# Optimization experiments

Measured on AMD Instinct MI355X. Metric: run time of the kernel, lower is better.

Reference implementation:

```python
import jax, jax.numpy as jnp
import numpy as np

N = 100_000   # nodes
E = 3_200_000 # edges (avg degree 32)
D = 256       # gnn width
H = 128       # mlp hidden
C = 5         # num classes


def _gcn_conv(x, W, b, src, dst, norm, n):
    # PyG GCNConv: h = x @ W^T, then symmetric-normalized scatter-add over edges
    h = x @ W.T
    msgs = norm[:, None] * h[src]                      # [E+N, out]
    out = jax.ops.segment_sum(msgs, dst, num_segments=n)
    return out + b


def setup_inputs() -> dict:
    key = jax.random.key(0)
    ks = jax.random.split(key, 8)
    x = jax.random.normal(ks[0], (N, D), dtype=jnp.float32)
    edge_index = jax.random.randint(ks[1], (2, E), 0, N, dtype=jnp.int32)
    def lin(k, out_d, in_d):
        return jax.random.normal(k, (out_d, in_d), dtype=jnp.float32) / np.sqrt(in_d).astype(np.float32)
    return {
        "x": x,
        "edge_index": edge_index,
        "W1": lin(ks[2], D, D), "b1": jnp.zeros((D,), jnp.float32),
        "W2": lin(ks[3], D, D), "b2": jnp.zeros((D,), jnp.float32),
        "Wm1": lin(ks[4], H, D), "bm1": jnp.zeros((H,), jnp.float32),
        "Wm2": lin(ks[5], C, H), "bm2": jnp.zeros((C,), jnp.float32),
    }


def reference(x, edge_index, W1, b1, W2, b2, Wm1, bm1, Wm2, bm2):
    # add self-loops (PyG GCNConv default add_self_loops=True)
    loop = jnp.arange(N, dtype=edge_index.dtype)
    src = jnp.concatenate([edge_index[0], loop])
    dst = jnp.concatenate([edge_index[1], loop])
    # symmetric normalization: deg from destination index (flow source_to_target)
    deg = jax.ops.segment_sum(jnp.ones(src.shape[0], x.dtype), dst, num_segments=N)
    dinv = jnp.where(deg > 0, jax.lax.rsqrt(deg), 0.0)
    norm = dinv[src] * dinv[dst]                       # [E+N]

    h = _gcn_conv(x, W1, b1, src, dst, norm, N)
    h = _gcn_conv(h, W2, b2, src, dst, norm, N)
    # MLP head (no activations in original module)
    h = h @ Wm1.T + bm1
    h = h @ Wm2.T + bm2
    return h
```

## Files before the change

### kernel.cpp

```cpp
#include <hip/hip_runtime.h>

#define N_NODES 100000
#define N_EDGES 3200000
#define DIM 256
#define HID 128
#define NCLS 5
#define BSH 8
#define BSZ 256
#define NBUCK 391
#define P1B 256
#define EPB 12500
#define HPKC 16

__global__ void k_zero(int* p, int n) {
    int i = blockIdx.x * 256 + threadIdx.x;
    if (i < n) p[i] = 0;
}

template<int K>
__global__ __launch_bounds__(256) void k_hp_stage(const float* __restrict__ A,
        const float* __restrict__ B, float* __restrict__ OUT)
{
    int t = threadIdx.x;
    int k0 = blockIdx.x * HPKC;
    float acc[NCLS] = {0, 0, 0, 0, 0};
    #pragma unroll
    for (int kk = 0; kk < HPKC; ++kk) {
        int k = k0 + kk;
        float b = B[k * DIM + t];
        #pragma unroll
        for (int c = 0; c < NCLS; ++c) acc[c] += A[c * K + k] * b;
    }
    #pragma unroll
    for (int c = 0; c < NCLS; ++c) unsafeAtomicAdd(&OUT[c * DIM + t], acc[c]);
}

__global__ __launch_bounds__(320) void k_hp_bias(const float* __restrict__ Wc,
        const float* __restrict__ W2c, const float* __restrict__ Wm2,
        const float* __restrict__ b1, const float* __restrict__ b2,
        const float* __restrict__ bm1, const float* __restrict__ bm2,
        float* __restrict__ bq, float* __restrict__ bc2)
{
    int c = threadIdx.x >> 6;
    int lane = threadIdx.x & 63;
    float s = 0.0f;
    for (int i = lane; i < DIM; i += 64) s += W2c[c * DIM + i] * b1[i];
    #pragma unroll
    for (int off = 32; off > 0; off >>= 1) s += __shfl_xor(s, off);
    float b = 0.0f;
    for (int k = lane; k < HID; k += 64) b += Wm2[c * HID + k] * bm1[k];
    for (int o = lane; o < DIM; o += 64) b += Wc[c * DIM + o] * b2[o];
    #pragma unroll
    for (int off = 32; off > 0; off >>= 1) b += __shfl_xor(b, off);
    if (lane == 0) { bq[c] = s; bc2[c] = bm2[c] + b; }
}

__global__ __launch_bounds__(1024) void k_p1hist(const int* __restrict__ dst,
        int* __restrict__ gcount, int* __restrict__ blockbase)
{
    __shared__ int lh[NBUCK];
    int tid = threadIdx.x;
    for (int i = tid; i < NBUCK; i += 1024) lh[i] = 0;
    __syncthreads();
    int s = blockIdx.x * EPB, e1 = s + EPB;
    for (int e = s + tid; e < e1; e += 1024) atomicAdd(&lh[dst[e] >> BSH], 1);
    __syncthreads();
    for (int i = tid; i < NBUCK; i += 1024) {
        int c = lh[i];
        blockbase[blockIdx.x * NBUCK + i] = c ? atomicAdd(&gcount[i], c) : 0;
    }
}
__global__ __launch_bounds__(512) void k_scanb(const int* __restrict__ gcount,
        int* __restrict__ gbase)
{
    __shared__ int sdata[512];
    int tid = threadIdx.x;
    int v = (tid < NBUCK) ? gcount[tid] : 0;
    sdata[tid] = v;
    __syncthreads();
    #pragma unroll
    for (int off = 1; off < 512; off <<= 1) {
        int t = (tid >= off) ? sdata[tid - off] : 0;
        __syncthreads();
        sdata[tid] += t;
        __syncthreads();
    }
    if (tid < NBUCK) gbase[tid] = sdata[tid] - v;
    if (tid == 0) gbase[NBUCK] = N_EDGES;
}
__global__ __launch_bounds__(1024) void k_p1scatter(const int* __restrict__ src,
        const int* __restrict__ dst, const int* __restrict__ gbase,
        const int* __restrict__ blockbase, unsigned* __restrict__ ebuf)
{
    __shared__ int lh[NBUCK];
    int tid = threadIdx.x;
    for (int i = tid; i < NBUCK; i += 1024) lh[i] = 0;
    __syncthreads();
    int s = blockIdx.x * EPB, e1 = s + EPB;
    for (int e = s + tid; e < e1; e += 1024) {
        int d = dst[e];
        int b = d >> BSH;
        int r = atomicAdd(&lh[b], 1);
        int pos = gbase[b] + blockbase[blockIdx.x * NBUCK + b] + r;
        ebuf[pos] = ((unsigned)src[e] << 8) | (unsigned)(d & 255);
    }
}
__global__ __launch_bounds__(512) void k_p2(const unsigned* __restrict__ ebuf,
        const int* __restrict__ gbase, int* __restrict__ rowptr,
        float* __restrict__ dinv, int* __restrict__ esrc)
{
    __shared__ int c[BSZ];
    __shared__ int sdata[BSZ];
    __shared__ int cur[BSZ];
    int tid = threadIdx.x, b = blockIdx.x;
    if (tid < BSZ) c[tid] = 0;
    __syncthreads();
    int s = gbase[b], e1 = gbase[b + 1];
    for (int e = s + tid; e < e1; e += 512) atomicAdd(&c[ebuf[e] & 255u], 1);
    __syncthreads();
    int cnt = (tid < BSZ) ? c[tid] : 0;
    if (tid < BSZ) sdata[tid] = cnt;
    __syncthreads();
    #pragma unroll
    for (int off = 1; off < BSZ; off <<= 1) {
        int t = (tid >= off && tid < BSZ) ? sdata[tid - off] : 0;
        __syncthreads();
        if (tid < BSZ) sdata[tid] += t;
        __syncthreads();
    }
    if (tid < BSZ) {
        int rp = s + sdata[tid] - cnt;
        cur[tid] = rp;
        int node = b * BSZ + tid;
        if (node < N_NODES) {
            rowptr[node] = rp;
            dinv[node] = rsqrtf((float)(cnt + 1));
        }
    }
    if (b == 0 && tid == 0) rowptr[N_NODES] = N_EDGES;
    __syncthreads();
    for (int e = s + tid; e < e1; e += 512) {
        unsigned p = ebuf[e];
        int pos = atomicAdd(&cur[p & 255u], 1);
        esrc[pos] = (int)(p >> 8);
    }
}

__global__ __launch_bounds__(256) void k_q(const float* __restrict__ x,
        const float* __restrict__ Wq, const float* __restrict__ dinv,
        float* __restrict__ qbuf)
{
    int wid = (blockIdx.x * 256 + threadIdx.x) >> 6;
    int lane = threadIdx.x & 63;
    int lane4 = lane * 4;
    int nwaves = gridDim.x * 4;
    float4 w[NCLS];
    #pragma unroll
    for (int c = 0; c < NCLS; ++c) w[c] = *(const float4*)(Wq + c * DIM + lane4);
    for (int d = wid; d < N_NODES; d += nwaves) {
        float4 xv = *(const float4*)(x + (size_t)d * DIM + lane4);
        float p[NCLS];
        #pragma unroll
        for (int c = 0; c < NCLS; ++c) {
            float s = xv.x * w[c].x + xv.y * w[c].y + xv.z * w[c].z + xv.w * w[c].w;
            #pragma unroll
            for (int off = 32; off > 0; off >>= 1) s += __shfl_xor(s, off);
            p[c] = s;
        }
        if (lane == 0) {
            float dv = dinv[d];
            #pragma unroll
            for (int c = 0; c < NCLS; ++c) qbuf[(size_t)d * 8 + c] = dv * p[c];
        }
    }
}

template<int MODE>
__global__ __launch_bounds__(256) void k_gather5(const float* __restrict__ in,
        const int* __restrict__ rowptr, const int* __restrict__ esrc,
        const float* __restrict__ dinv, const float* __restrict__ bias,
        float* __restrict__ out, int ostride)
{
    int gid = blockIdx.x * 256 + threadIdx.x;
    int d = gid >> 2, sub = gid & 3;
    if (d >= N_NODES) return;
    float acc0 = 0, acc1 = 0, acc2 = 0, acc3 = 0, acc4 = 0;
    int r0 = rowptr[d], r1 = rowptr[d + 1];
    for (int j = r0 + sub; j < r1; j += 4) {
        int s = esrc[j];
        float4 v = *(const float4*)(in + (size_t)s * 8);
        float v4 = in[(size_t)s * 8 + 4];
        acc0 += v.x; acc1 += v.y; acc2 += v.z; acc3 += v.w; acc4 += v4;
    }
    if (sub == 0) {
        float4 v = *(const float4*)(in + (size_t)d * 8);
        float v4 = in[(size_t)d * 8 + 4];
        acc0 += v.x; acc1 += v.y; acc2 += v.z; acc3 += v.w; acc4 += v4;
    }
    #pragma unroll
    for (int off = 1; off < 4; off <<= 1) {
        acc0 += __shfl_xor(acc0, off);
        acc1 += __shfl_xor(acc1, off);
        acc2 += __shfl_xor(acc2, off);
        acc3 += __shfl_xor(acc3, off);
        acc4 += __shfl_xor(acc4, off);
    }
    if (sub == 0) {
        float dv = dinv[d];
        float sc = (MODE == 1) ? dv * dv : dv;
        float bs = (MODE == 1) ? dv : 1.0f;
        out[(size_t)d * ostride + 0] = sc * acc0 + bs * bias[0];
        out[(size_t)d * ostride + 1] = sc * acc1 + bs * bias[1];
        out[(size_t)d * ostride + 2] = sc * acc2 + bs * bias[2];
        out[(size_t)d * ostride + 3] = sc * acc3 + bs * bias[3];
        out[(size_t)d * ostride + 4] = sc * acc4 + bs * bias[4];
    }
}

extern "C" void kernel_launch(void* const* d_in, const int* in_sizes, int n_in,
                              void* d_out, int out_size, void* d_ws, size_t ws_size,
                              hipStream_t stream)
{
    const float* x   = (const float*)d_in[0];
    const int*   ei  = (const int*)d_in[1];
    const float* W1  = (const float*)d_in[2];
    const float* b1  = (const float*)d_in[3];
    const float* W2  = (const float*)d_in[4];
    const float* b2  = (const float*)d_in[5];
    const float* Wm1 = (const float*)d_in[6];
    const float* bm1 = (const float*)d_in[7];
    const float* Wm2 = (const float*)d_in[8];
    const float* bm2 = (const float*)d_in[9];
    float* out = (float*)d_out;
    const int* src = ei;
    const int* dst = ei + N_EDGES;

    char* ws = (char*)d_ws;
    float* dinv     = (float*)   (ws + 0x0000000);
    int* rowptr     = (int*)     (ws + 0x0080000);
    int* esrc       = (int*)     (ws + 0x0200000);
    float* hpw      = (float*)   (ws + 0x0F00000);
    float* Wq       = hpw;
    float* Wc       = hpw + NCLS * DIM;
    float* W2c      = hpw + 2 * NCLS * DIM;
    int* gcount     = (int*)     (hpw + 3 * NCLS * DIM);
    float* bq       = (float*)   (ws + 0x0F10000);
    float* bc2      = (float*)   (ws + 0x0F11000);
    float* qbuf     = (float*)   (ws + 0x1000000);
    float* tbuf     = (float*)   (ws + 0x1400000);
    unsigned* ebuf  = (unsigned*)(ws + 0x1800000);
    int* blockbase  = (int*)     (ws + 0x2600000);
    int* gbase      = (int*)     (ws + 0x2700000);

    const int NZ = 3 * NCLS * DIM + NBUCK;
    k_zero<<<(NZ + 255) / 256, 256, 0, stream>>>((int*)hpw, NZ);

    k_hp_stage<HID><<<HID / HPKC, 256, 0, stream>>>(Wm2, Wm1, Wc);
    k_hp_stage<DIM><<<DIM / HPKC, 256, 0, stream>>>(Wc, W2, W2c);
    k_hp_bias<<<1, 320, 0, stream>>>(Wc, W2c, Wm2, b1, b2, bm1, bm2, bq, bc2);
    k_hp_stage<DIM><<<DIM / HPKC, 256, 0, stream>>>(W2c, W1, Wq);

    k_p1hist<<<P1B, 1024, 0, stream>>>(dst, gcount, blockbase);
    k_scanb<<<1, 512, 0, stream>>>(gcount, gbase);
    k_p1scatter<<<P1B, 1024, 0, stream>>>(src, dst, gbase, blockbase, ebuf);
    k_p2<<<NBUCK, 512, 0, stream>>>(ebuf, gbase, rowptr, dinv, esrc);

    k_q<<<2048, 256, 0, stream>>>(x, Wq, dinv, qbuf);

    const int GB = (N_NODES * 4 + 255) / 256;
    k_gather5<1><<<GB, 256, 0, stream>>>(qbuf, rowptr, esrc, dinv, bq, tbuf, 8);
    k_gather5<0><<<GB, 256, 0, stream>>>(tbuf, rowptr, esrc, dinv, bc2, out, NCLS);
}
```

Before: 330.9 us.

## Merge bias and Wq weight kernels, widen p2 blocks, unroll gather by two

The bias computation and the final weight-product stage now share one launch, with the extra block computing the biases, which removes one kernel launch. The bucket-sort second pass now runs 1024 threads per block instead of 512 to get more parallelism per bucket. The 5-wide gather loop is unrolled twice so two neighbor loads are in flight per iteration. The effects are small and independent, and p2 still runs only 391 blocks.

```diff
diff --git a/kernel.cpp b/kernel.cpp
--- a/kernel.cpp
+++ b/kernel.cpp
@@ -35,24 +35,41 @@
     for (int c = 0; c < NCLS; ++c) unsafeAtomicAdd(&OUT[c * DIM + t], acc[c]);
 }
 
-__global__ __launch_bounds__(320) void k_hp_bias(const float* __restrict__ Wc,
-        const float* __restrict__ W2c, const float* __restrict__ Wm2,
+__global__ __launch_bounds__(256) void k_hp_final(const float* __restrict__ W2c,
+        const float* __restrict__ W1, float* __restrict__ Wq,
+        const float* __restrict__ Wc, const float* __restrict__ Wm2,
         const float* __restrict__ b1, const float* __restrict__ b2,
         const float* __restrict__ bm1, const float* __restrict__ bm2,
         float* __restrict__ bq, float* __restrict__ bc2)
 {
-    int c = threadIdx.x >> 6;
-    int lane = threadIdx.x & 63;
-    float s = 0.0f;
-    for (int i = lane; i < DIM; i += 64) s += W2c[c * DIM + i] * b1[i];
-    #pragma unroll
-    for (int off = 32; off > 0; off >>= 1) s += __shfl_xor(s, off);
-    float b = 0.0f;
-    for (int k = lane; k < HID; k += 64) b += Wm2[c * HID + k] * bm1[k];
-    for (int o = lane; o < DIM; o += 64) b += Wc[c * DIM + o] * b2[o];
-    #pragma unroll
-    for (int off = 32; off > 0; off >>= 1) b += __shfl_xor(b, off);
-    if (lane == 0) { bq[c] = s; bc2[c] = bm2[c] + b; }
+    if (blockIdx.x < DIM / HPKC) {
+        int t = threadIdx.x;
+        int k0 = blockIdx.x * HPKC;
+        float acc[NCLS] = {0, 0, 0, 0, 0};
+        #pragma unroll
+        for (int kk = 0; kk < HPKC; ++kk) {
+            int k = k0 + kk;
+            float b = W1[k * DIM + t];
+            #pragma unroll
+            for (int c = 0; c < NCLS; ++c) acc[c] += W2c[c * DIM + k] * b;
+        }
+        #pragma unroll
+        for (int c = 0; c < NCLS; ++c) unsafeAtomicAdd(&Wq[c * DIM + t], acc[c]);
+    } else {
+        int w = threadIdx.x >> 6, lane = threadIdx.x & 63;
+        for (int c = w; c < NCLS; c += 4) {
+            float s = 0.0f;
+            for (int i = lane; i < DIM; i += 64) s += W2c[c * DIM + i] * b1[i];
+            #pragma unroll
+            for (int off = 32; off > 0; off >>= 1) s += __shfl_xor(s, off);
+            float bsum = 0.0f;
+            for (int k = lane; k < HID; k += 64) bsum += Wm2[c * HID + k] * bm1[k];
+            for (int o = lane; o < DIM; o += 64) bsum += Wc[c * DIM + o] * b2[o];
+            #pragma unroll
+            for (int off = 32; off > 0; off >>= 1) bsum += __shfl_xor(bsum, off);
+            if (lane == 0) { bq[c] = s; bc2[c] = bm2[c] + bsum; }
+        }
+    }
 }
 
 __global__ __launch_bounds__(1024) void k_p1hist(const int* __restrict__ dst,
@@ -105,7 +122,7 @@
         ebuf[pos] = ((unsigned)src[e] << 8) | (unsigned)(d & 255);
     }
 }
-__global__ __launch_bounds__(512) void k_p2(const unsigned* __restrict__ ebuf,
+__global__ __launch_bounds__(1024) void k_p2(const unsigned* __restrict__ ebuf,
         const int* __restrict__ gbase, int* __restrict__ rowptr,
         float* __restrict__ dinv, int* __restrict__ esrc)
 {
@@ -116,7 +133,7 @@
     if (tid < BSZ) c[tid] = 0;
     __syncthreads();
     int s = gbase[b], e1 = gbase[b + 1];
-    for (int e = s + tid; e < e1; e += 512) atomicAdd(&c[ebuf[e] & 255u], 1);
+    for (int e = s + tid; e < e1; e += 1024) atomicAdd(&c[ebuf[e] & 255u], 1);
     __syncthreads();
     int cnt = (tid < BSZ) ? c[tid] : 0;
     if (tid < BSZ) sdata[tid] = cnt;
@@ -139,7 +156,7 @@
     }
     if (b == 0 && tid == 0) rowptr[N_NODES] = N_EDGES;
     __syncthreads();
-    for (int e = s + tid; e < e1; e += 512) {
+    for (int e = s + tid; e < e1; e += 1024) {
         unsigned p = ebuf[e];
         int pos = atomicAdd(&cur[p & 255u], 1);
         esrc[pos] = (int)(p >> 8);
@@ -186,7 +203,18 @@
     if (d >= N_NODES) return;
     float acc0 = 0, acc1 = 0, acc2 = 0, acc3 = 0, acc4 = 0;
     int r0 = rowptr[d], r1 = rowptr[d + 1];
-    for (int j = r0 + sub; j < r1; j += 4) {
+    int j = r0 + sub;
+    for (; j + 4 < r1; j += 8) {
+        int s0 = esrc[j];
+        int s1 = esrc[j + 4];
+        float4 v0 = *(const float4*)(in + (size_t)s0 * 8);
+        float a0 = in[(size_t)s0 * 8 + 4];
+        float4 v1 = *(const float4*)(in + (size_t)s1 * 8);
+        float a1 = in[(size_t)s1 * 8 + 4];
+        acc0 += v0.x + v1.x; acc1 += v0.y + v1.y; acc2 += v0.z + v1.z;
+        acc3 += v0.w + v1.w; acc4 += a0 + a1;
+    }
+    for (; j < r1; j += 4) {
         int s = esrc[j];
         float4 v = *(const float4*)(in + (size_t)s * 8);
         float v4 = in[(size_t)s * 8 + 4];
@@ -257,13 +285,13 @@
 
     k_hp_stage<HID><<<HID / HPKC, 256, 0, stream>>>(Wm2, Wm1, Wc);
     k_hp_stage<DIM><<<DIM / HPKC, 256, 0, stream>>>(Wc, W2, W2c);
-    k_hp_bias<<<1, 320, 0, stream>>>(Wc, W2c, Wm2, b1, b2, bm1, bm2, bq, bc2);
-    k_hp_stage<DIM><<<DIM / HPKC, 256, 0, stream>>>(W2c, W1, Wq);
+    k_hp_final<<<DIM / HPKC + 1, 256, 0, stream>>>(W2c, W1, Wq,
+            Wc, Wm2, b1, b2, bm1, bm2, bq, bc2);
 
     k_p1hist<<<P1B, 1024, 0, stream>>>(dst, gcount, blockbase);
     k_scanb<<<1, 512, 0, stream>>>(gcount, gbase);
     k_p1scatter<<<P1B, 1024, 0, stream>>>(src, dst, gbase, blockbase, ebuf);
-    k_p2<<<NBUCK, 512, 0, stream>>>(ebuf, gbase, rowptr, dinv, esrc);
+    k_p2<<<NBUCK, 1024, 0, stream>>>(ebuf, gbase, rowptr, dinv, esrc);
 
     k_q<<<2048, 256, 0, stream>>>(x, Wq, dinv, qbuf);
 
```

Result: faster. 323.0 us (-2.4%).
